# Kernel tuning notes

Measured on AMD Instinct MI355X. Metric: run time of the kernel, lower is better.

Reference implementation:

```python
import jax, jax.numpy as jnp
import numpy as np

B, S, D, H = 16, 1024, 768, 12
HS = D // H  # head size = 64
NEG = -1000000.0  # module uses -1e6, not -inf


def setup_inputs() -> dict:
    key = jax.random.key(0)
    k1, k2, k3 = jax.random.split(key, 3)
    scale = 1.0 / np.sqrt(D)
    return {
        "x": jax.random.normal(k1, (B, S, D), dtype=jnp.float32),
        "W_qkv": jax.random.normal(k2, (D, 3 * D), dtype=jnp.float32) * scale,
        "b_qkv": jnp.zeros((3 * D,), dtype=jnp.float32),
        "W_o": jax.random.normal(k3, (D, D), dtype=jnp.float32) * scale,
        "b_o": jnp.zeros((D,), dtype=jnp.float32),
    }


def reference(x, W_qkv, b_qkv, W_o, b_o):
    qkv = x @ W_qkv + b_qkv                      # [B,S,3D]
    q, k, v = jnp.split(qkv, 3, axis=-1)         # each [B,S,D]
    q = q.reshape(B, S, H, HS)
    k = k.reshape(B, S, H, HS)
    v = v.reshape(B, S, H, HS)
    scores = jnp.einsum('bqhd,bkhd->bhqk', q, k) / np.sqrt(HS).astype(np.float32)
    causal = jnp.tril(jnp.ones((S, S), dtype=bool))
    scores = jnp.where(causal, scores, jnp.float32(NEG))
    probs = jax.nn.softmax(scores, axis=-1)      # dropout is eval-mode identity
    av = jnp.einsum('bhqk,bkhd->bqhd', probs, v).reshape(B, S, D)
    return av @ W_o + b_o
```

## Files before the change

kernel.cpp:

```cpp
#include <hip/hip_runtime.h>
#include <stdint.h>

typedef unsigned short u16;
typedef __attribute__((ext_vector_type(8))) short bf16x8;
typedef __attribute__((ext_vector_type(8))) u16 u16x8;
typedef __attribute__((ext_vector_type(4))) u16 u16x4;
typedef __attribute__((ext_vector_type(4))) float f32x4;
typedef __attribute__((ext_vector_type(16))) float f32x16;

#define B_ 16
#define S_ 1024
#define D_ 768
#define H_ 12

__device__ __forceinline__ float bf2f(u16 u) {
  unsigned int x = ((unsigned int)u) << 16;
  float f;
  __builtin_memcpy(&f, &x, 4);
  return f;
}
__device__ __forceinline__ u16 f2bf(float f) {
  unsigned int x;
  __builtin_memcpy(&x, &f, 4);
  x += 0x7fffu + ((x >> 16) & 1u);
  return (u16)(x >> 16);
}

#define MFMA16(a, b, c) __builtin_amdgcn_mfma_f32_16x16x32_bf16((a), (b), (c), 0, 0, 0)
#define MFMA32(a, b, c) __builtin_amdgcn_mfma_f32_32x32x16_bf16((a), (b), (c), 0, 0, 0)

#define GLD16(g, l)                                              \
  __builtin_amdgcn_global_load_lds(                              \
      (const __attribute__((address_space(1))) void*)(g),        \
      (__attribute__((address_space(3))) void*)(l), 16, 0, 0)

__global__ __launch_bounds__(256) void prep(const float* __restrict__ x,
                                            u16* __restrict__ xb,
                                            const float* __restrict__ Wqkv,
                                            u16* __restrict__ WqkvT,
                                            const float* __restrict__ Wo,
                                            u16* __restrict__ WoT) {
  __shared__ u16 tt[32][33];
  const int gx = blockIdx.x;
  const int tid = threadIdx.x;
  if (gx < 6144) {
    const int i = gx * 256 + tid;
    const float4 a = *(const float4*)(x + (size_t)i * 8);
    const float4 b = *(const float4*)(x + (size_t)i * 8 + 4);
    u16x8 o;
    o[0] = f2bf(a.x); o[1] = f2bf(a.y); o[2] = f2bf(a.z); o[3] = f2bf(a.w);
    o[4] = f2bf(b.x); o[5] = f2bf(b.y); o[6] = f2bf(b.z); o[7] = f2bf(b.w);
    *(u16x8*)(xb + (size_t)i * 8) = o;
  } else if (gx < 6144 + 1728) {
    const int t = gx - 6144;
    const int n0 = (t % 72) * 32, k0 = (t / 72) * 32;
    const int tx = tid & 31, ty = tid >> 5;
#pragma unroll
    for (int i = 0; i < 32; i += 8)
      tt[ty + i][tx] = f2bf(Wqkv[(size_t)(k0 + ty + i) * 2304 + n0 + tx]);
    __syncthreads();
#pragma unroll
    for (int i = 0; i < 32; i += 8)
      WqkvT[(size_t)(n0 + ty + i) * 768 + k0 + tx] = tt[tx][ty + i];
  } else {
    const int t = gx - 7872;
    const int n0 = (t % 24) * 32, k0 = (t / 24) * 32;
    const int tx = tid & 31, ty = tid >> 5;
#pragma unroll
    for (int i = 0; i < 32; i += 8)
      tt[ty + i][tx] = f2bf(Wo[(size_t)(k0 + ty + i) * 768 + n0 + tx]);
    __syncthreads();
#pragma unroll
    for (int i = 0; i < 32; i += 8)
      WoT[(size_t)(n0 + ty + i) * 768 + k0 + tx] = tt[tx][ty + i];
  }
}

template <int MODE>
__global__ __launch_bounds__(256, 2) void gemm_bt(const u16* __restrict__ A,
                                                  const u16* __restrict__ Bt,
                                                  const float* __restrict__ bias,
                                                  u16* __restrict__ O0, u16* __restrict__ O1,
                                                  u16* __restrict__ O2, float* __restrict__ Of,
                                                  int M, int N, int K, int NBT) {
  __shared__ u16 Al[2 * 128 * 64];
  __shared__ u16 Bl[2 * 128 * 64];
  const int tid = threadIdx.x;
  const int wid = tid >> 6, lane = tid & 63;
  const int lo = lane & 15, hi = lane >> 4;
  const int wr = wid >> 1, wc = wid & 1;
  const int bid = blockIdx.x;
  const int xcd = bid & 7, idx = bid >> 3;
  const int mb = xcd * 16 + idx / NBT;
  const int nb = idx % NBT;
  const int m0 = mb * 128, n0 = nb * 128;
  const int T = K >> 6;

  const int sr = lane >> 3;
  const int kk = ((lane & 7) ^ sr) * 8;
  const u16* const asrc = A + (size_t)(m0 + wid * 8 + sr) * K + kk;
  const u16* const bsrc = Bt + (size_t)(n0 + wid * 8 + sr) * K + kk;

#define STAGE(kt, buf)                                                          \
  do {                                                                          \
    const size_t _k = (size_t)(kt) * 64;                                        \
    GLD16(asrc + _k, (char*)Al + (buf) * 16384 + (wid) * 1024);                 \
    GLD16(asrc + (size_t)32 * K + _k, (char*)Al + (buf) * 16384 + (wid + 4) * 1024);  \
    GLD16(asrc + (size_t)64 * K + _k, (char*)Al + (buf) * 16384 + (wid + 8) * 1024);  \
    GLD16(asrc + (size_t)96 * K + _k, (char*)Al + (buf) * 16384 + (wid + 12) * 1024); \
    GLD16(bsrc + _k, (char*)Bl + (buf) * 16384 + (wid) * 1024);                 \
    GLD16(bsrc + (size_t)32 * K + _k, (char*)Bl + (buf) * 16384 + (wid + 4) * 1024);  \
    GLD16(bsrc + (size_t)64 * K + _k, (char*)Bl + (buf) * 16384 + (wid + 8) * 1024);  \
    GLD16(bsrc + (size_t)96 * K + _k, (char*)Bl + (buf) * 16384 + (wid + 12) * 1024); \
  } while (0)

  f32x4 acc[4][4] = {};

  STAGE(0, 0);
  asm volatile("s_waitcnt vmcnt(0)" ::: "memory");
  __builtin_amdgcn_s_barrier();

  for (int t = 0; t < T; ++t) {
    if (t + 1 < T) STAGE(t + 1, (t + 1) & 1);
    const int cb = (t & 1) * 16384;
    const int swz = (lo & 7) << 4;
    bf16x8 af[4][2], bfv[4][2];
#pragma unroll
    for (int i = 0; i < 4; ++i)
#pragma unroll
      for (int s = 0; s < 2; ++s)
        af[i][s] = *(const bf16x8*)((const char*)Al + cb + (wr * 64 + i * 16 + lo) * 128 +
                                    ((s * 64 + hi * 16) ^ swz));
#pragma unroll
    for (int j = 0; j < 4; ++j)
#pragma unroll
      for (int s = 0; s < 2; ++s)
        bfv[j][s] = *(const bf16x8*)((const char*)Bl + cb + (wc * 64 + j * 16 + lo) * 128 +
                                     ((s * 64 + hi * 16) ^ swz));
    __builtin_amdgcn_s_setprio(1);
#pragma unroll
    for (int i = 0; i < 4; ++i)
#pragma unroll
      for (int j = 0; j < 4; ++j) {
        acc[i][j] = MFMA16(af[i][0], bfv[j][0], acc[i][j]);
        acc[i][j] = MFMA16(af[i][1], bfv[j][1], acc[i][j]);
      }
    __builtin_amdgcn_s_setprio(0);
    if (t + 1 < T) asm volatile("s_waitcnt vmcnt(0)" ::: "memory");
    __builtin_amdgcn_s_barrier();
  }
#undef STAGE
  if (MODE == 0 && n0 >= 2 * D_) {
#pragma unroll
    for (int g = 0; g < 4; ++g) {
      const int n = n0 + wc * 64 + g * 16 + lo;
      const float bv = bias[n];
      const int np = n - 2 * D_;
#pragma unroll
      for (int f = 0; f < 4; ++f) {
        const int m = m0 + wr * 64 + f * 16 + hi * 4;
        u16x4 q;
#pragma unroll
        for (int r = 0; r < 4; ++r) q[r] = f2bf(acc[f][g][r] + bv);
        *(u16x4*)&O2[(((size_t)(m >> 10) * H_ + (np >> 6)) * 64 + (np & 63)) * S_ +
                     (m & 1023)] = q;
      }
    }
  } else {
#pragma unroll
    for (int g = 0; g < 4; ++g) {
      const int n = n0 + wc * 64 + g * 16 + lo;
      const float bv = bias[n];
#pragma unroll
      for (int f = 0; f < 4; ++f) {
#pragma unroll
        for (int r = 0; r < 4; ++r) {
          const int m = m0 + wr * 64 + f * 16 + hi * 4 + r;
          const float fv = acc[f][g][r] + bv;
          if (MODE == 0) {
            const u16 o = f2bf(fv);
            if (n0 < D_) {
              O0[(size_t)m * D_ + n] = o;
            } else {
              O1[(size_t)m * D_ + (n - D_)] = o;
            }
          } else {
            Of[(size_t)m * N + n] = fv;
          }
        }
      }
    }
  }
}

__global__ __launch_bounds__(256) void attn_fwd2(const u16* __restrict__ Qb,
                                                 const u16* __restrict__ Kb,
                                                 const u16* __restrict__ VTb,
                                                 u16* __restrict__ att) {
  __shared__ u16 Kl[2048];
  __shared__ u16 Vl[2048];
  const int tid = threadIdx.x;
  const int lane = tid & 63, wid = tid >> 6;
  const int l31 = lane & 31, hi1 = lane >> 5;
  const int L = blockIdx.x + 8 * (blockIdx.y + 12 * blockIdx.z);
  const int bx = (L >> 3) & 7;
  const int P = (L & 7) + 8 * (L >> 6);
  const int h = P % 12, b = P / 12;
  const int q0 = bx * 128;
  const int qw0 = q0 + wid * 32;
  const int qg = qw0 + l31;
  const size_t rowbase = (size_t)b * S_;

  bf16x8 qf[4];
  {
    const u16* qp = Qb + (rowbase + qg) * D_ + h * 64 + hi1 * 8;
#pragma unroll
    for (int c = 0; c < 4; ++c) {
      bf16x8 v = *(const bf16x8*)(qp + c * 16);
#pragma unroll
      for (int j = 0; j < 8; ++j) v[j] = (short)f2bf(bf2f((u16)v[j]) * 0.125f);
      qf[c] = v;
    }
  }
  float mrun = -3.0e38f, lrun = 0.0f;
  f32x16 o0 = {}, o1 = {};

  const u16* kgp =
      Kb + (rowbase + (tid & 31)) * D_ + h * 64 + (tid >> 6) * 16 + ((tid >> 5) & 1) * 8;
  const u16* vgp = VTb +
                   (((size_t)b * H_ + h) * 64 + ((tid >> 6) & 1) * 32 + (tid & 31)) * S_ +
                   (tid >> 7) * 16 + ((tid >> 5) & 1) * 8;
  char* kdst = (char*)Kl + wid * 1024;
  char* vdst = (char*)Vl + wid * 1024;
  const char* kbase = (const char*)Kl + lane * 16;
  const char* vbase = (const char*)Vl + lane * 16;

  const int kvend = q0 + 128;
  for (int kv0 = 0; kv0 < kvend; kv0 += 32) {
    __syncthreads();
    GLD16(kgp + (size_t)kv0 * D_, kdst);
    GLD16(vgp + kv0, vdst);
    __syncthreads();
    if (kv0 > qw0 + 31) continue;

    f32x16 s = {};
#pragma unroll
    for (int c = 0; c < 4; ++c) s = MFMA32(*(const bf16x8*)(kbase + c * 1024), qf[c], s);

    if (kv0 + 31 > qw0) {
#pragma unroll
      for (int r = 0; r < 16; ++r) {
        const int kvg = kv0 + (r & 3) + 8 * (r >> 2) + 4 * hi1;
        if (kvg > qg) s[r] = -1.0e30f;
      }
    }
    float rm = s[0];
#pragma unroll
    for (int r = 1; r < 16; ++r) rm = fmaxf(rm, s[r]);
    rm = fmaxf(rm, __shfl_xor(rm, 32));
    const float mn = fmaxf(mrun, rm);
    const float fr = __expf(mrun - mn);
    mrun = mn;
    float p[16];
    float rs = 0.0f;
#pragma unroll
    for (int r = 0; r < 16; ++r) {
      p[r] = __expf(s[r] - mn);
      rs += p[r];
    }
    rs += __shfl_xor(rs, 32);
    lrun = lrun * fr + rs;
#pragma unroll
    for (int r = 0; r < 16; ++r) {
      o0[r] *= fr;
      o1[r] *= fr;
    }
    unsigned int pa[4], pb[4];
#pragma unroll
    for (int g = 0; g < 4; ++g) {
      pa[g] = (unsigned)f2bf(p[4 * g]) | ((unsigned)f2bf(p[4 * g + 1]) << 16);
      pb[g] = (unsigned)f2bf(p[4 * g + 2]) | ((unsigned)f2bf(p[4 * g + 3]) << 16);
    }
    const unsigned sa = __shfl_xor(hi1 ? pa[0] : pa[1], 32);
    const unsigned sb = __shfl_xor(hi1 ? pb[0] : pb[1], 32);
    const unsigned sc = __shfl_xor(hi1 ? pa[2] : pa[3], 32);
    const unsigned sd = __shfl_xor(hi1 ? pb[2] : pb[3], 32);
    const uint4 w0 = hi1 ? make_uint4(sa, sb, pa[1], pb[1]) : make_uint4(pa[0], pb[0], sa, sb);
    const uint4 w1 = hi1 ? make_uint4(sc, sd, pa[3], pb[3]) : make_uint4(pa[2], pb[2], sc, sd);
    bf16x8 pf0, pf1;
    __builtin_memcpy(&pf0, &w0, 16);
    __builtin_memcpy(&pf1, &w1, 16);
    o0 = MFMA32(*(const bf16x8*)(vbase + 0 * 1024), pf0, o0);
    o1 = MFMA32(*(const bf16x8*)(vbase + 1 * 1024), pf0, o1);
    o0 = MFMA32(*(const bf16x8*)(vbase + 2 * 1024), pf1, o0);
    o1 = MFMA32(*(const bf16x8*)(vbase + 3 * 1024), pf1, o1);
  }
  const float inv = 1.0f / lrun;
  u16* op = att + (rowbase + qg) * D_ + h * 64;
#pragma unroll
  for (int g = 0; g < 4; ++g) {
    u16x4 v0, v1;
#pragma unroll
    for (int j = 0; j < 4; ++j) {
      v0[j] = f2bf(o0[4 * g + j] * inv);
      v1[j] = f2bf(o1[4 * g + j] * inv);
    }
    *(u16x4*)(op + 8 * g + 4 * hi1) = v0;
    *(u16x4*)(op + 32 + 8 * g + 4 * hi1) = v1;
  }
}

extern "C" void kernel_launch(void* const* d_in, const int* in_sizes, int n_in, void* d_out,
                              int out_size, void* d_ws, size_t ws_size, hipStream_t stream) {
  const float *x = nullptr, *Wqkv = nullptr, *bqkv = nullptr, *Wo = nullptr, *bo = nullptr;
  for (int i = 0; i < n_in; ++i) {
    switch (in_sizes[i]) {
      case 16384 * 768:  x = (const float*)d_in[i]; break;
      case 768 * 2304:   Wqkv = (const float*)d_in[i]; break;
      case 2304:         bqkv = (const float*)d_in[i]; break;
      case 768 * 768:    Wo = (const float*)d_in[i]; break;
      case 768:          bo = (const float*)d_in[i]; break;
    }
  }
  float* out = (float*)d_out;

  char* ws = (char*)d_ws;
  u16* WqkvT = (u16*)(ws);
  u16* WoT = (u16*)(ws + 3538944);
  u16* Qb = (u16*)(ws + 4718592);
  u16* Kb = (u16*)(ws + 29884416);
  u16* VT = (u16*)(ws + 55050240);
  u16* xb = (u16*)d_out;
  u16* att = Qb;

  prep<<<8448, 256, 0, stream>>>(x, xb, Wqkv, WqkvT, Wo, WoT);
  gemm_bt<0><<<2304, 256, 0, stream>>>(xb, WqkvT, bqkv, Qb, Kb, VT, nullptr,
                                       16384, 2304, 768, 18);
  attn_fwd2<<<dim3(8, H_, B_), 256, 0, stream>>>(Qb, Kb, VT, att);
  gemm_bt<1><<<768, 256, 0, stream>>>(att, WoT, bo, nullptr, nullptr, nullptr, out,
                                      16384, 768, 768, 6);
}
```

Baseline: 239.7 us.

## Double-buffer K/V tiles in attention, skip rescale, pack bf16, reverse block order

The attention kernel now double-buffers its K/V tiles in LDS. The next tile's global-to-LDS load is issued before computing on the current one, so each iteration needs one barrier instead of two. It also skips the online-softmax rescale unless the running max grows by more than a threshold, uses the hardware packed bf16 conversion instruction, and schedules the heavier causal query blocks first to reduce tail imbalance. LDS use doubles. The lazy rescale lets exponentials grow by up to e^8 before renormalization, which slightly changes numerics.

```diff
diff --git a/kernel.cpp b/kernel.cpp
--- a/kernel.cpp
+++ b/kernel.cpp
@@ -24,6 +24,11 @@
   __builtin_memcpy(&x, &f, 4);
   x += 0x7fffu + ((x >> 16) & 1u);
   return (u16)(x >> 16);
+}
+__device__ __forceinline__ unsigned cvt_pk_bf16(float lo, float hi) {
+  unsigned r;
+  asm("v_cvt_pk_bf16_f32 %0, %1, %2" : "=v"(r) : "v"(lo), "v"(hi));
+  return r;
 }
 
 #define MFMA16(a, b, c) __builtin_amdgcn_mfma_f32_16x16x32_bf16((a), (b), (c), 0, 0, 0)
@@ -193,17 +198,17 @@
   }
 }
 
-__global__ __launch_bounds__(256) void attn_fwd2(const u16* __restrict__ Qb,
+__global__ __launch_bounds__(256) void attn_fwd3(const u16* __restrict__ Qb,
                                                  const u16* __restrict__ Kb,
                                                  const u16* __restrict__ VTb,
                                                  u16* __restrict__ att) {
-  __shared__ u16 Kl[2048];
-  __shared__ u16 Vl[2048];
+  __shared__ u16 Kl[2 * 2048];
+  __shared__ u16 Vl[2 * 2048];
   const int tid = threadIdx.x;
   const int lane = tid & 63, wid = tid >> 6;
   const int l31 = lane & 31, hi1 = lane >> 5;
   const int L = blockIdx.x + 8 * (blockIdx.y + 12 * blockIdx.z);
-  const int bx = (L >> 3) & 7;
+  const int bx = 7 - ((L >> 3) & 7);
   const int P = (L & 7) + 8 * (L >> 6);
   const int h = P % 12, b = P / 12;
   const int q0 = bx * 128;
@@ -230,70 +235,87 @@
   const u16* vgp = VTb +
                    (((size_t)b * H_ + h) * 64 + ((tid >> 6) & 1) * 32 + (tid & 31)) * S_ +
                    (tid >> 7) * 16 + ((tid >> 5) & 1) * 8;
-  char* kdst = (char*)Kl + wid * 1024;
-  char* vdst = (char*)Vl + wid * 1024;
-  const char* kbase = (const char*)Kl + lane * 16;
-  const char* vbase = (const char*)Vl + lane * 16;
-
-  const int kvend = q0 + 128;
-  for (int kv0 = 0; kv0 < kvend; kv0 += 32) {
-    __syncthreads();
-    GLD16(kgp + (size_t)kv0 * D_, kdst);
-    GLD16(vgp + kv0, vdst);
-    __syncthreads();
-    if (kv0 > qw0 + 31) continue;
-
-    f32x16 s = {};
-#pragma unroll
-    for (int c = 0; c < 4; ++c) s = MFMA32(*(const bf16x8*)(kbase + c * 1024), qf[c], s);
-
-    if (kv0 + 31 > qw0) {
+  char* const kdst = (char*)Kl + wid * 1024;
+  char* const vdst = (char*)Vl + wid * 1024;
+  const char* const kbase = (const char*)Kl + lane * 16;
+  const char* const vbase = (const char*)Vl + lane * 16;
+
+  const int T = (q0 + 128) >> 5;
+
+  GLD16(kgp, kdst);
+  GLD16(vgp, vdst);
+  asm volatile("s_waitcnt vmcnt(0)" ::: "memory");
+  __builtin_amdgcn_s_barrier();
+
+  for (int t = 0; t < T; ++t) {
+    const int kv0 = t * 32;
+    if (t + 1 < T) {
+      const int nb = ((t + 1) & 1) * 4096;
+      GLD16(kgp + (size_t)(t + 1) * 32 * D_, kdst + nb);
+      GLD16(vgp + (t + 1) * 32, vdst + nb);
+    }
+    if (kv0 <= qw0 + 31) {
+      const int cb = (t & 1) * 4096;
+      f32x16 s = {};
+#pragma unroll
+      for (int c = 0; c < 4; ++c)
+        s = MFMA32(*(const bf16x8*)(kbase + cb + c * 1024), qf[c], s);
+
+      if (kv0 + 31 > qw0) {
+#pragma unroll
+        for (int r = 0; r < 16; ++r) {
+          const int kvg = kv0 + (r & 3) + 8 * (r >> 2) + 4 * hi1;
+          if (kvg > qg) s[r] = -1.0e30f;
+        }
+      }
+      float rm = s[0];
+#pragma unroll
+      for (int r = 1; r < 16; ++r) rm = fmaxf(rm, s[r]);
+      rm = fmaxf(rm, __shfl_xor(rm, 32));
+      if (!__all(rm - mrun <= 8.0f)) {
+        const float mn = fmaxf(mrun, rm);
+        const float fr = __expf(mrun - mn);
+        mrun = mn;
+        lrun *= fr;
+#pragma unroll
+        for (int r = 0; r < 16; ++r) {
+          o0[r] *= fr;
+          o1[r] *= fr;
+        }
+      }
+      float p[16];
+      float rs = 0.0f;
 #pragma unroll
       for (int r = 0; r < 16; ++r) {
-        const int kvg = kv0 + (r & 3) + 8 * (r >> 2) + 4 * hi1;
-        if (kvg > qg) s[r] = -1.0e30f;
-      }
-    }
-    float rm = s[0];
-#pragma unroll
-    for (int r = 1; r < 16; ++r) rm = fmaxf(rm, s[r]);
-    rm = fmaxf(rm, __shfl_xor(rm, 32));
-    const float mn = fmaxf(mrun, rm);
-    const float fr = __expf(mrun - mn);
-    mrun = mn;
-    float p[16];
-    float rs = 0.0f;
-#pragma unroll
-    for (int r = 0; r < 16; ++r) {
-      p[r] = __expf(s[r] - mn);
-      rs += p[r];
-    }
-    rs += __shfl_xor(rs, 32);
-    lrun = lrun * fr + rs;
-#pragma unroll
-    for (int r = 0; r < 16; ++r) {
-      o0[r] *= fr;
-      o1[r] *= fr;
-    }
-    unsigned int pa[4], pb[4];
-#pragma unroll
-    for (int g = 0; g < 4; ++g) {
-      pa[g] = (unsigned)f2bf(p[4 * g]) | ((unsigned)f2bf(p[4 * g + 1]) << 16);
-      pb[g] = (unsigned)f2bf(p[4 * g + 2]) | ((unsigned)f2bf(p[4 * g + 3]) << 16);
-    }
-    const unsigned sa = __shfl_xor(hi1 ? pa[0] : pa[1], 32);
-    const unsigned sb = __shfl_xor(hi1 ? pb[0] : pb[1], 32);
-    const unsigned sc = __shfl_xor(hi1 ? pa[2] : pa[3], 32);
-    const unsigned sd = __shfl_xor(hi1 ? pb[2] : pb[3], 32);
-    const uint4 w0 = hi1 ? make_uint4(sa, sb, pa[1], pb[1]) : make_uint4(pa[0], pb[0], sa, sb);
-    const uint4 w1 = hi1 ? make_uint4(sc, sd, pa[3], pb[3]) : make_uint4(pa[2], pb[2], sc, sd);
-    bf16x8 pf0, pf1;
-    __builtin_memcpy(&pf0, &w0, 16);
-    __builtin_memcpy(&pf1, &w1, 16);
-    o0 = MFMA32(*(const bf16x8*)(vbase + 0 * 1024), pf0, o0);
-    o1 = MFMA32(*(const bf16x8*)(vbase + 1 * 1024), pf0, o1);
-    o0 = MFMA32(*(const bf16x8*)(vbase + 2 * 1024), pf1, o0);
-    o1 = MFMA32(*(const bf16x8*)(vbase + 3 * 1024), pf1, o1);
+        p[r] = __expf(s[r] - mrun);
+        rs += p[r];
+      }
+      rs += __shfl_xor(rs, 32);
+      lrun += rs;
+      unsigned int pa[4], pb[4];
+#pragma unroll
+      for (int g = 0; g < 4; ++g) {
+        pa[g] = cvt_pk_bf16(p[4 * g], p[4 * g + 1]);
+        pb[g] = cvt_pk_bf16(p[4 * g + 2], p[4 * g + 3]);
+      }
+      const unsigned sa = __shfl_xor(hi1 ? pa[0] : pa[1], 32);
+      const unsigned sb = __shfl_xor(hi1 ? pb[0] : pb[1], 32);
+      const unsigned sc = __shfl_xor(hi1 ? pa[2] : pa[3], 32);
+      const unsigned sd = __shfl_xor(hi1 ? pb[2] : pb[3], 32);
+      const uint4 w0 =
+          hi1 ? make_uint4(sa, sb, pa[1], pb[1]) : make_uint4(pa[0], pb[0], sa, sb);
+      const uint4 w1 =
+          hi1 ? make_uint4(sc, sd, pa[3], pb[3]) : make_uint4(pa[2], pb[2], sc, sd);
+      bf16x8 pf0, pf1;
+      __builtin_memcpy(&pf0, &w0, 16);
+      __builtin_memcpy(&pf1, &w1, 16);
+      o0 = MFMA32(*(const bf16x8*)(vbase + cb + 0 * 1024), pf0, o0);
+      o1 = MFMA32(*(const bf16x8*)(vbase + cb + 1 * 1024), pf0, o1);
+      o0 = MFMA32(*(const bf16x8*)(vbase + cb + 2 * 1024), pf1, o0);
+      o1 = MFMA32(*(const bf16x8*)(vbase + cb + 3 * 1024), pf1, o1);
+    }
+    asm volatile("s_waitcnt vmcnt(0)" ::: "memory");
+    __builtin_amdgcn_s_barrier();
   }
   const float inv = 1.0f / lrun;
   u16* op = att + (rowbase + qg) * D_ + h * 64;
@@ -336,7 +358,7 @@
   prep<<<8448, 256, 0, stream>>>(x, xb, Wqkv, WqkvT, Wo, WoT);
   gemm_bt<0><<<2304, 256, 0, stream>>>(xb, WqkvT, bqkv, Qb, Kb, VT, nullptr,
                                        16384, 2304, 768, 18);
-  attn_fwd2<<<dim3(8, H_, B_), 256, 0, stream>>>(Qb, Kb, VT, att);
+  attn_fwd3<<<dim3(8, H_, B_), 256, 0, stream>>>(Qb, Kb, VT, att);
   gemm_bt<1><<<768, 256, 0, stream>>>(att, WoT, bo, nullptr, nullptr, nullptr, out,
                                       16384, 768, 768, 6);
 }
```

After: 222.1 us. 7.3% less time.
